# Performance work log

Hardware: AMD Instinct MI355X
Metric: run time of the kernel (lower is better)

The kernel has to match this reference:

```python
import jax, jax.numpy as jnp
import numpy as np

N = 10000       # nodes
E = 640000      # edges
D_IN = 128
D_OUT = 128
EPS = 1e-5      # LayerNorm eps (torch default)


def setup_inputs() -> dict:
    key = jax.random.key(0)
    k_x, k_e, k_w, k_b, k_g = jax.random.split(key, 5)
    x = jax.random.normal(k_x, (N, D_IN), dtype=jnp.float32)
    edge_index = jax.random.randint(k_e, (2, E), 0, N, dtype=jnp.int64)
    # GCNConv linear weight (PyG uses glorot) and bias
    lim = float(np.sqrt(6.0 / (D_IN + D_OUT)))
    W = jax.random.uniform(k_w, (D_IN, D_OUT), minval=-lim, maxval=lim, dtype=jnp.float32)
    b = jnp.zeros((D_OUT,), dtype=jnp.float32)
    # LayerNorm affine params
    gamma = jnp.ones((D_OUT,), dtype=jnp.float32)
    beta = jnp.zeros((D_OUT,), dtype=jnp.float32)
    return {"x": x, "edge_index": edge_index, "W": W, "b": b, "gamma": gamma, "beta": beta}


def reference(x, edge_index, W, b, gamma, beta):
    # --- GCNConv: A_hat = D^{-1/2} (A + I) D^{-1/2}; out = A_hat X W + b ---
    self_idx = jnp.arange(N, dtype=edge_index.dtype)
    src = jnp.concatenate([edge_index[0], self_idx])  # [E+N]
    dst = jnp.concatenate([edge_index[1], self_idx])  # [E+N]
    deg = jax.ops.segment_sum(jnp.ones_like(src, dtype=x.dtype), dst, num_segments=N)
    dinv = jnp.where(deg > 0, jax.lax.rsqrt(deg), 0.0)  # [N]
    norm = dinv[src] * dinv[dst]                        # [E+N]
    h = x @ W                                           # [N, D_OUT] transform first (cheaper)
    msg = h[src] * norm[:, None]                        # [E+N, D_OUT]
    out = jax.ops.segment_sum(msg, dst, num_segments=N) + b
    # --- LayerNorm over feature dim ---
    mu = jnp.mean(out, axis=-1, keepdims=True)
    var = jnp.mean(jnp.square(out - mu), axis=-1, keepdims=True)
    out = (out - mu) * jax.lax.rsqrt(var + EPS) * gamma + beta
    # act = Identity (last_act=ReLU is truthy -> Identity branch); dropout = eval identity; residual=False
    return out
```

## Files before the change

kernel.cpp:

```cpp
#include <hip/hip_runtime.h>
#include <hip/hip_fp16.h>

#define D 128
#define LN_EPS 1e-5f


static __device__ __forceinline__ float h2f(unsigned short h) {
    return __half2float(__builtin_bit_cast(__half, h));
}
static __device__ __forceinline__ unsigned short f2h(float f) {
    return __builtin_bit_cast(unsigned short, __float2half_rn(f));
}

static __device__ __forceinline__ void flagbar(int* slots, int c, int C, int phase) {
    __syncthreads();
    int val = 0x5A5A0001 + phase;
    int tid = threadIdx.x;
    if (tid == 0)
        __hip_atomic_store(&slots[phase * 64 + c], val, __ATOMIC_RELEASE, __HIP_MEMORY_SCOPE_AGENT);
    if (tid < C) {
        while (__hip_atomic_load(&slots[phase * 64 + tid], __ATOMIC_ACQUIRE, __HIP_MEMORY_SCOPE_AGENT) != val)
            __builtin_amdgcn_s_sleep(1);
    }
    __syncthreads();
}

__global__ __launch_bounds__(1024) void build_kernel(
        const int* __restrict__ src, const int* __restrict__ dst,
        const float* __restrict__ x, const float* __restrict__ W,
        unsigned int* __restrict__ xh, unsigned int* __restrict__ Wh,
        unsigned short* __restrict__ ghist, int* __restrict__ blocksum,
        int* __restrict__ rowptr, float* __restrict__ dinv,
        unsigned short* __restrict__ csr, int* __restrict__ bar,
        int N, int E, int Ec, int NH, int NW, int C) {
    extern __shared__ int lds[];
    __shared__ int s_scan[20];
    int c = blockIdx.x;
    int tid = threadIdx.x;
    int lane = tid & 63, wv = tid >> 6;

    for (int i = tid; i < N; i += 1024) lds[i] = 0;
    int gs = gridDim.x * 1024;
    int tot = NH + NW;
    for (int i = c * 1024 + tid; i < tot; i += gs) {
        if (i < NH) {
            float2 v = ((const float2*)x)[i];
            xh[i] = (unsigned int)f2h(v.x) | ((unsigned int)f2h(v.y) << 16);
        } else {
            float2 v = ((const float2*)W)[i - NH];
            Wh[i - NH] = (unsigned int)f2h(v.x) | ((unsigned int)f2h(v.y) << 16);
        }
    }
    __syncthreads();
    int lo = c * Ec, hi = min(lo + Ec, E);
    #pragma unroll 4
    for (int i = lo + tid; i < hi; i += 1024)
        atomicAdd(&lds[dst[i]], 1);
    __syncthreads();
    for (int i = tid; i < N; i += 1024)
        ghist[(size_t)c * N + i] = (unsigned short)lds[i];
    flagbar(bar, c, C, 0);

    int nper = (N + C - 1) / C;
    int n0 = c * nper;
    int nn = min(nper, N - n0); if (nn < 0) nn = 0;
    int mydeg = 0;
    if (tid < nn) {
        int n = n0 + tid;
        int run = 0;
        #pragma unroll 8
        for (int cc = 0; cc < C; cc++) {
            int t = ghist[(size_t)cc * N + n];
            ghist[(size_t)cc * N + n] = (unsigned short)run;
            run += t;
        }
        mydeg = run;
        dinv[n] = rsqrtf((float)(run + 1));
    }
    int incl = mydeg;
    #pragma unroll
    for (int off = 1; off < 64; off <<= 1) {
        int y = __shfl_up(incl, off);
        if (lane >= off) incl += y;
    }
    if (lane == 63) s_scan[wv] = incl;
    __syncthreads();
    if (tid == 0) {
        int run = 0;
        #pragma unroll
        for (int k = 0; k < 16; k++) { int t = s_scan[k]; s_scan[k] = run; run += t; }
        blocksum[c] = run;
    }
    __syncthreads();
    if (tid < nn) rowptr[n0 + tid] = s_scan[wv] + incl - mydeg;
    flagbar(bar, c, C, 1);

    if (tid < 64) {
        int bs = (tid < C) ? blocksum[tid] : 0;
        int inc2 = bs;
        #pragma unroll
        for (int off = 1; off < 64; off <<= 1) {
            int y = __shfl_up(inc2, off);
            if (tid >= off) inc2 += y;
        }
        if (tid == c)     s_scan[18] = inc2 - bs;
        if (tid == C - 1) s_scan[19] = inc2;
    }
    __syncthreads();
    int base = s_scan[18];
    if (tid < nn) rowptr[n0 + tid] += base;
    if (c == C - 1 && tid == 0) rowptr[N] = s_scan[19];
    flagbar(bar, c, C, 2);

    for (int i = tid; i < N; i += 1024)
        lds[i] = rowptr[i] + ghist[(size_t)c * N + i];
    __syncthreads();
    #pragma unroll 4
    for (int i = lo + tid; i < hi; i += 1024) {
        int d = dst[i];
        int pos = atomicAdd(&lds[d], 1);
        csr[pos] = (unsigned short)src[i];
    }
}

__global__ __launch_bounds__(512) void fused_fp16(const unsigned int* __restrict__ xh,
                                                  const unsigned int* __restrict__ Wh,
                                                  const int* __restrict__ rowptr,
                                                  const unsigned short* __restrict__ csr,
                                                  const float* __restrict__ dinv,
                                                  const float* __restrict__ bias,
                                                  const float* __restrict__ gamma,
                                                  const float* __restrict__ beta,
                                                  float* __restrict__ out, int N) {
    int w = threadIdx.x >> 6, lane = threadIdx.x & 63;
    int node = blockIdx.x * 8 + w;
    if (node >= N) return;
    float dn = dinv[node];

    unsigned int xv = xh[node * 64 + lane];
    float a0 = h2f((unsigned short)xv) * dn * dn;
    float a1 = h2f((unsigned short)(xv >> 16)) * dn * dn;

    int start = rowptr[node], end = rowptr[node + 1];
    int base = start;
    for (; base + 64 <= end; base += 64) {
        int s = csr[base + lane];
        float wt = dinv[s] * dn;
        #pragma unroll 8
        for (int k = 0; k < 64; k++) {
            int sk = __shfl(s, k);
            float wk = __shfl(wt, k);
            unsigned int hv = xh[sk * 64 + lane];
            a0 += h2f((unsigned short)hv) * wk;
            a1 += h2f((unsigned short)(hv >> 16)) * wk;
        }
    }
    int rem = end - base;
    if (rem > 0) {
        int s = 0; float wt = 0.f;
        if (lane < rem) { s = csr[base + lane]; wt = dinv[s] * dn; }
        for (int k = 0; k < rem; k++) {
            int sk = __shfl(s, k);
            float wk = __shfl(wt, k);
            unsigned int hv = xh[sk * 64 + lane];
            a0 += h2f((unsigned short)hv) * wk;
            a1 += h2f((unsigned short)(hv >> 16)) * wk;
        }
    }

    int c0 = lane * 2;
    float y0 = bias[c0], y1 = bias[c0 + 1];
    #pragma unroll 8
    for (int k = 0; k < 64; k++) {
        float g0 = __shfl(a0, k);
        float g1 = __shfl(a1, k);
        unsigned int w0 = Wh[(2 * k) * 64 + lane];
        unsigned int w1 = Wh[(2 * k + 1) * 64 + lane];
        y0 += g0 * h2f((unsigned short)w0) + g1 * h2f((unsigned short)w1);
        y1 += g0 * h2f((unsigned short)(w0 >> 16)) + g1 * h2f((unsigned short)(w1 >> 16));
    }

    float sum = y0 + y1, sq = y0 * y0 + y1 * y1;
    #pragma unroll
    for (int off = 32; off > 0; off >>= 1) {
        sum += __shfl_xor(sum, off);
        sq  += __shfl_xor(sq, off);
    }
    float mean = sum * (1.0f / D);
    float var  = sq * (1.0f / D) - mean * mean;
    float inv  = rsqrtf(var + LN_EPS);
    float o0 = (y0 - mean) * inv * gamma[c0] + beta[c0];
    float o1 = (y1 - mean) * inv * gamma[c0 + 1] + beta[c0 + 1];
    *(float2*)(out + (size_t)node * D + c0) = make_float2(o0, o1);
}


__global__ void deg_kernel(const int* __restrict__ dst, int* __restrict__ deg, int E) {
    int e = blockIdx.x * blockDim.x + threadIdx.x;
    if (e < E) atomicAdd(&deg[dst[e]], 1);
}
__global__ __launch_bounds__(1024) void scan_kernel(const int* __restrict__ deg,
                                                    int* __restrict__ rowptr,
                                                    int* __restrict__ fill,
                                                    float* __restrict__ dinv, int N) {
    __shared__ int s_wsum[16];
    __shared__ int s_woff[16];
    __shared__ int s_carry;
    int t = threadIdx.x;
    int lane = t & 63, w = t >> 6;
    if (t == 0) s_carry = 0;
    __syncthreads();
    for (int base = 0; base < N; base += 1024) {
        int i = base + t;
        int v = (i < N) ? deg[i] : 0;
        int incl = v;
        #pragma unroll
        for (int off = 1; off < 64; off <<= 1) {
            int y = __shfl_up(incl, off);
            if (lane >= off) incl += y;
        }
        if (lane == 63) s_wsum[w] = incl;
        __syncthreads();
        if (t == 0) {
            int run = s_carry;
            #pragma unroll
            for (int k = 0; k < 16; k++) { s_woff[k] = run; run += s_wsum[k]; }
            s_carry = run;
        }
        __syncthreads();
        if (i < N) {
            int rp = s_woff[w] + (incl - v);
            rowptr[i] = rp;
            fill[i] = rp;
            dinv[i] = rsqrtf((float)(v + 1));
        }
    }
    if (t == 0) rowptr[N] = s_carry;
}
__global__ void fill_kernel(const int* __restrict__ src, const int* __restrict__ dst,
                            int* __restrict__ fill, unsigned short* __restrict__ csr, int E) {
    int e = blockIdx.x * blockDim.x + threadIdx.x;
    if (e < E) {
        int pos = atomicAdd(&fill[dst[e]], 1);
        csr[pos] = (unsigned short)src[e];
    }
}
__global__ __launch_bounds__(512) void fused_fp32(const float* __restrict__ x,
                                                  const float* __restrict__ W,
                                                  const int* __restrict__ rowptr,
                                                  const unsigned short* __restrict__ csr,
                                                  const float* __restrict__ dinv,
                                                  const float* __restrict__ bias,
                                                  const float* __restrict__ gamma,
                                                  const float* __restrict__ beta,
                                                  float* __restrict__ out, int N) {
    __shared__ float sW[D * D];
    {
        const float4* Wv = (const float4*)W;
        float4* sWv = (float4*)sW;
        #pragma unroll
        for (int i = 0; i < (D * D / 4) / 512; i++)
            sWv[threadIdx.x + i * 512] = Wv[threadIdx.x + i * 512];
    }
    __syncthreads();
    int w = threadIdx.x >> 6, lane = threadIdx.x & 63;
    int node = blockIdx.x * 8 + w;
    if (node >= N) return;
    float dn = dinv[node];
    int c0 = lane * 2;
    float2 xv = *(const float2*)(x + (size_t)node * D + c0);
    float a0 = xv.x * dn * dn, a1 = xv.y * dn * dn;
    int start = rowptr[node], end = rowptr[node + 1];
    int base = start;
    for (; base + 64 <= end; base += 64) {
        int s = csr[base + lane];
        float wt = dinv[s] * dn;
        #pragma unroll 8
        for (int k = 0; k < 64; k++) {
            int sk = __shfl(s, k);
            float wk = __shfl(wt, k);
            float2 xs = *(const float2*)(x + (size_t)sk * D + c0);
            a0 += xs.x * wk; a1 += xs.y * wk;
        }
    }
    int rem = end - base;
    if (rem > 0) {
        int s = 0; float wt = 0.f;
        if (lane < rem) { s = csr[base + lane]; wt = dinv[s] * dn; }
        for (int k = 0; k < rem; k++) {
            int sk = __shfl(s, k);
            float wk = __shfl(wt, k);
            float2 xs = *(const float2*)(x + (size_t)sk * D + c0);
            a0 += xs.x * wk; a1 += xs.y * wk;
        }
    }
    float y0 = bias[c0], y1 = bias[c0 + 1];
    #pragma unroll 8
    for (int k = 0; k < 64; k++) {
        float g0 = __shfl(a0, k);
        float g1 = __shfl(a1, k);
        float2 w0 = *(const float2*)(sW + (2 * k) * D + c0);
        float2 w1 = *(const float2*)(sW + (2 * k + 1) * D + c0);
        y0 += g0 * w0.x + g1 * w1.x;
        y1 += g0 * w0.y + g1 * w1.y;
    }
    float sum = y0 + y1, sq = y0 * y0 + y1 * y1;
    #pragma unroll
    for (int off = 32; off > 0; off >>= 1) {
        sum += __shfl_xor(sum, off);
        sq  += __shfl_xor(sq, off);
    }
    float mean = sum * (1.0f / D);
    float var  = sq * (1.0f / D) - mean * mean;
    float inv  = rsqrtf(var + LN_EPS);
    float o0 = (y0 - mean) * inv * gamma[c0] + beta[c0];
    float o1 = (y1 - mean) * inv * gamma[c0 + 1] + beta[c0 + 1];
    *(float2*)(out + (size_t)node * D + c0) = make_float2(o0, o1);
}

extern "C" void kernel_launch(void* const* d_in, const int* in_sizes, int n_in,
                              void* d_out, int out_size, void* d_ws, size_t ws_size,
                              hipStream_t stream) {
    const float* x     = (const float*)d_in[0];
    const int*   ei    = (const int*)d_in[1];
    const float* W     = (const float*)d_in[2];
    const float* bias  = (const float*)d_in[3];
    const float* gamma = (const float*)d_in[4];
    const float* beta  = (const float*)d_in[5];
    float*       out   = (float*)d_out;

    int N = in_sizes[0] / D;
    int E = in_sizes[1] / 2;
    const int* src = ei;
    const int* dst = ei + E;

    char* ws = (char*)d_ws;
    size_t off = 0;
    auto carve = [&](size_t bytes) { size_t p = off; off = (off + bytes + 15) & ~15UL; return (void*)(ws + p); };
    int*            bar      = (int*)           carve(3 * 64 * 4);
    int*            blocksum = (int*)           carve(64 * 4);
    int*            rowptr   = (int*)           carve((size_t)(N + 1) * 4);
    float*          dinv     = (float*)         carve((size_t)N * 4);
    unsigned short* csr      = (unsigned short*)carve((size_t)E * 2);
    unsigned int*   xh       = (unsigned int*)  carve((size_t)N * (D / 2) * 4);
    unsigned int*   Wh       = (unsigned int*)  carve((size_t)D * (D / 2) * 4);
    size_t fixed_end = off;

    int C = 0;
    if (ws_size > fixed_end + 16) {
        size_t avail = ws_size - fixed_end - 16;
        size_t cmax = avail / ((size_t)N * 2);
        C = (int)((cmax > 64) ? 64 : cmax);
    }

    if (C >= 16) {
        unsigned short* ghist = (unsigned short*)carve((size_t)C * N * 2);
        int Ec = (E + C - 1) / C;
        int NH = N * (D / 2);
        int NW = D * (D / 2);
        size_t lds = (size_t)N * 4;
        build_kernel<<<C, 1024, lds, stream>>>(src, dst, x, W, xh, Wh, ghist,
                                               blocksum, rowptr, dinv, csr, bar,
                                               N, E, Ec, NH, NW, C);
        fused_fp16<<<(N + 7) / 8, 512, 0, stream>>>(xh, Wh, rowptr, csr, dinv,
                                                    bias, gamma, beta, out, N);
    } else {
        int* deg  = (int*)carve((size_t)N * 4);
        int* fill = (int*)carve((size_t)N * 4);
        hipMemsetAsync(deg, 0, (size_t)N * 4, stream);
        deg_kernel<<<(E + 255) / 256, 256, 0, stream>>>(dst, deg, E);
        scan_kernel<<<1, 1024, 0, stream>>>(deg, rowptr, fill, dinv, N);
        fill_kernel<<<(E + 255) / 256, 256, 0, stream>>>(src, dst, fill, csr, E);
        fused_fp32<<<(N + 7) / 8, 512, 0, stream>>>(x, W, rowptr, csr, dinv,
                                                    bias, gamma, beta, out, N);
    }
}
```

Measured before the change: 152.4 us.

## Replace per-block LDS histograms with global atomics across 256-block persistent grid

Rewrites the CSR build kernel to drop the per-block LDS degree histograms and the two-level distributed scan. It launches 256 blocks that count degrees with global atomics, lets a single block scan the degrees, then fills the CSR using global atomics on a fill array. The aim is to use more of the GPU in the build phase and to remove the ghist traffic and extra scan stages. In exchange it adds global-atomic contention, a serial single-block scan over N nodes, and a spin barrier across 256 blocks, which assumes all blocks are resident at once.

```diff
diff --git a/kernel.cpp b/kernel.cpp
--- a/kernel.cpp
+++ b/kernel.cpp
@@ -12,37 +12,40 @@
     return __builtin_bit_cast(unsigned short, __float2half_rn(f));
 }
 
-static __device__ __forceinline__ void flagbar(int* slots, int c, int C, int phase) {
+#define NBAR_SLOTS 256
+
+static __device__ __forceinline__ void flagbar(int* slots, int c, int G, int phase) {
     __syncthreads();
     int val = 0x5A5A0001 + phase;
     int tid = threadIdx.x;
     if (tid == 0)
-        __hip_atomic_store(&slots[phase * 64 + c], val, __ATOMIC_RELEASE, __HIP_MEMORY_SCOPE_AGENT);
-    if (tid < C) {
-        while (__hip_atomic_load(&slots[phase * 64 + tid], __ATOMIC_ACQUIRE, __HIP_MEMORY_SCOPE_AGENT) != val)
+        __hip_atomic_store(&slots[phase * NBAR_SLOTS + c], val, __ATOMIC_RELEASE, __HIP_MEMORY_SCOPE_AGENT);
+    if (tid < G) {
+        while (__hip_atomic_load(&slots[phase * NBAR_SLOTS + tid], __ATOMIC_ACQUIRE, __HIP_MEMORY_SCOPE_AGENT) != val)
             __builtin_amdgcn_s_sleep(1);
     }
     __syncthreads();
 }
 
-__global__ __launch_bounds__(1024) void build_kernel(
+__global__ __launch_bounds__(1024) void build2_kernel(
         const int* __restrict__ src, const int* __restrict__ dst,
         const float* __restrict__ x, const float* __restrict__ W,
         unsigned int* __restrict__ xh, unsigned int* __restrict__ Wh,
-        unsigned short* __restrict__ ghist, int* __restrict__ blocksum,
-        int* __restrict__ rowptr, float* __restrict__ dinv,
+        int* __restrict__ deg, int* __restrict__ rowptr,
+        int* __restrict__ fill, float* __restrict__ dinv,
         unsigned short* __restrict__ csr, int* __restrict__ bar,
-        int N, int E, int Ec, int NH, int NW, int C) {
-    extern __shared__ int lds[];
-    __shared__ int s_scan[20];
+        int N, int E, int NH, int NW, int G) {
+    __shared__ int s_wsum[16];
+    __shared__ int s_woff[16];
+    __shared__ int s_carry;
     int c = blockIdx.x;
     int tid = threadIdx.x;
-    int lane = tid & 63, wv = tid >> 6;
-
-    for (int i = tid; i < N; i += 1024) lds[i] = 0;
-    int gs = gridDim.x * 1024;
+    int gs = G * 1024;
+    int g0 = c * 1024 + tid;
+
+    for (int i = g0; i < N; i += gs) deg[i] = 0;
     int tot = NH + NW;
-    for (int i = c * 1024 + tid; i < tot; i += gs) {
+    for (int i = g0; i < tot; i += gs) {
         if (i < NH) {
             float2 v = ((const float2*)x)[i];
             xh[i] = (unsigned int)f2h(v.x) | ((unsigned int)f2h(v.y) << 16);
@@ -51,74 +54,50 @@
             Wh[i - NH] = (unsigned int)f2h(v.x) | ((unsigned int)f2h(v.y) << 16);
         }
     }
-    __syncthreads();
-    int lo = c * Ec, hi = min(lo + Ec, E);
-    #pragma unroll 4
-    for (int i = lo + tid; i < hi; i += 1024)
-        atomicAdd(&lds[dst[i]], 1);
-    __syncthreads();
-    for (int i = tid; i < N; i += 1024)
-        ghist[(size_t)c * N + i] = (unsigned short)lds[i];
-    flagbar(bar, c, C, 0);
-
-    int nper = (N + C - 1) / C;
-    int n0 = c * nper;
-    int nn = min(nper, N - n0); if (nn < 0) nn = 0;
-    int mydeg = 0;
-    if (tid < nn) {
-        int n = n0 + tid;
-        int run = 0;
-        #pragma unroll 8
-        for (int cc = 0; cc < C; cc++) {
-            int t = ghist[(size_t)cc * N + n];
-            ghist[(size_t)cc * N + n] = (unsigned short)run;
-            run += t;
-        }
-        mydeg = run;
-        dinv[n] = rsqrtf((float)(run + 1));
-    }
-    int incl = mydeg;
-    #pragma unroll
-    for (int off = 1; off < 64; off <<= 1) {
-        int y = __shfl_up(incl, off);
-        if (lane >= off) incl += y;
-    }
-    if (lane == 63) s_scan[wv] = incl;
-    __syncthreads();
-    if (tid == 0) {
-        int run = 0;
-        #pragma unroll
-        for (int k = 0; k < 16; k++) { int t = s_scan[k]; s_scan[k] = run; run += t; }
-        blocksum[c] = run;
-    }
-    __syncthreads();
-    if (tid < nn) rowptr[n0 + tid] = s_scan[wv] + incl - mydeg;
-    flagbar(bar, c, C, 1);
-
-    if (tid < 64) {
-        int bs = (tid < C) ? blocksum[tid] : 0;
-        int inc2 = bs;
-        #pragma unroll
-        for (int off = 1; off < 64; off <<= 1) {
-            int y = __shfl_up(inc2, off);
-            if (tid >= off) inc2 += y;
-        }
-        if (tid == c)     s_scan[18] = inc2 - bs;
-        if (tid == C - 1) s_scan[19] = inc2;
-    }
-    __syncthreads();
-    int base = s_scan[18];
-    if (tid < nn) rowptr[n0 + tid] += base;
-    if (c == C - 1 && tid == 0) rowptr[N] = s_scan[19];
-    flagbar(bar, c, C, 2);
-
-    for (int i = tid; i < N; i += 1024)
-        lds[i] = rowptr[i] + ghist[(size_t)c * N + i];
-    __syncthreads();
-    #pragma unroll 4
-    for (int i = lo + tid; i < hi; i += 1024) {
-        int d = dst[i];
-        int pos = atomicAdd(&lds[d], 1);
+    flagbar(bar, c, G, 0);
+
+    #pragma unroll 2
+    for (int i = g0; i < E; i += gs)
+        atomicAdd(&deg[dst[i]], 1);
+    flagbar(bar, c, G, 1);
+
+    if (c == 0) {
+        int lane = tid & 63, w = tid >> 6;
+        if (tid == 0) s_carry = 0;
+        __syncthreads();
+        for (int base = 0; base < N; base += 1024) {
+            int i = base + tid;
+            int v = (i < N) ? deg[i] : 0;
+            int incl = v;
+            #pragma unroll
+            for (int off = 1; off < 64; off <<= 1) {
+                int y = __shfl_up(incl, off);
+                if (lane >= off) incl += y;
+            }
+            if (lane == 63) s_wsum[w] = incl;
+            __syncthreads();
+            if (tid == 0) {
+                int run = s_carry;
+                #pragma unroll
+                for (int k = 0; k < 16; k++) { s_woff[k] = run; run += s_wsum[k]; }
+                s_carry = run;
+            }
+            __syncthreads();
+            if (i < N) {
+                int rp = s_woff[w] + (incl - v);
+                rowptr[i] = rp;
+                fill[i] = rp;
+                dinv[i] = rsqrtf((float)(v + 1));
+            }
+        }
+        if (tid == 0) rowptr[N] = s_carry;
+    }
+    flagbar(bar, c, G, 2);
+
+    #pragma unroll 2
+    for (int i = g0; i < E; i += gs) {
+        int d_ = dst[i];
+        int pos = atomicAdd(&fill[d_], 1);
         csr[pos] = (unsigned short)src[i];
     }
 }
@@ -337,36 +316,27 @@
     char* ws = (char*)d_ws;
     size_t off = 0;
     auto carve = [&](size_t bytes) { size_t p = off; off = (off + bytes + 15) & ~15UL; return (void*)(ws + p); };
-    int*            bar      = (int*)           carve(3 * 64 * 4);
-    int*            blocksum = (int*)           carve(64 * 4);
-    int*            rowptr   = (int*)           carve((size_t)(N + 1) * 4);
-    float*          dinv     = (float*)         carve((size_t)N * 4);
-    unsigned short* csr      = (unsigned short*)carve((size_t)E * 2);
-    unsigned int*   xh       = (unsigned int*)  carve((size_t)N * (D / 2) * 4);
-    unsigned int*   Wh       = (unsigned int*)  carve((size_t)D * (D / 2) * 4);
-    size_t fixed_end = off;
-
-    int C = 0;
-    if (ws_size > fixed_end + 16) {
-        size_t avail = ws_size - fixed_end - 16;
-        size_t cmax = avail / ((size_t)N * 2);
-        C = (int)((cmax > 64) ? 64 : cmax);
-    }
-
-    if (C >= 16) {
-        unsigned short* ghist = (unsigned short*)carve((size_t)C * N * 2);
-        int Ec = (E + C - 1) / C;
+    int*            bar    = (int*)           carve(3 * NBAR_SLOTS * 4);
+    int*            rowptr = (int*)           carve((size_t)(N + 1) * 4);
+    float*          dinv   = (float*)         carve((size_t)N * 4);
+    int*            deg    = (int*)           carve((size_t)N * 4);
+    int*            fill   = (int*)           carve((size_t)N * 4);
+    unsigned short* csr    = (unsigned short*)carve((size_t)E * 2);
+    size_t fallback_end = off;
+    unsigned int*   xh     = (unsigned int*)  carve((size_t)N * (D / 2) * 4);
+    unsigned int*   Wh     = (unsigned int*)  carve((size_t)D * (D / 2) * 4);
+    size_t full_end = off;
+
+    if (full_end <= ws_size && N <= 65535) {
+        int G = 256;
         int NH = N * (D / 2);
         int NW = D * (D / 2);
-        size_t lds = (size_t)N * 4;
-        build_kernel<<<C, 1024, lds, stream>>>(src, dst, x, W, xh, Wh, ghist,
-                                               blocksum, rowptr, dinv, csr, bar,
-                                               N, E, Ec, NH, NW, C);
+        build2_kernel<<<G, 1024, 0, stream>>>(src, dst, x, W, xh, Wh,
+                                              deg, rowptr, fill, dinv, csr, bar,
+                                              N, E, NH, NW, G);
         fused_fp16<<<(N + 7) / 8, 512, 0, stream>>>(xh, Wh, rowptr, csr, dinv,
                                                     bias, gamma, beta, out, N);
-    } else {
-        int* deg  = (int*)carve((size_t)N * 4);
-        int* fill = (int*)carve((size_t)N * 4);
+    } else if (fallback_end <= ws_size) {
         hipMemsetAsync(deg, 0, (size_t)N * 4, stream);
         deg_kernel<<<(E + 255) / 256, 256, 0, stream>>>(dst, deg, E);
         scan_kernel<<<1, 1024, 0, stream>>>(deg, rowptr, fill, dinv, N);
```

Result: slower. 281.0 us (+84.5%).

## Transform features before aggregation and fold source normalization into prescaled H

Applied to the files above, without the earlier changes.

The dense transform now runs first, as a separate GEMM kernel that computes H = X·W, scales each row by dinv[src] and stores it as fp16. The aggregation kernel then just sums the prescaled H rows over the CSR neighbors and multiplies by dinv[dst]. This removes the per-edge dinv gather and multiply and drops the per-node GEMM from the fused kernel. The costs are an extra kernel launch, an fp16 round trip of H, and rounding after the product instead of before it.

```diff
diff --git a/kernel.cpp b/kernel.cpp
--- a/kernel.cpp
+++ b/kernel.cpp
@@ -27,12 +27,11 @@
 
 __global__ __launch_bounds__(1024) void build_kernel(
         const int* __restrict__ src, const int* __restrict__ dst,
-        const float* __restrict__ x, const float* __restrict__ W,
-        unsigned int* __restrict__ xh, unsigned int* __restrict__ Wh,
+        const float* __restrict__ W, unsigned int* __restrict__ Wh,
         unsigned short* __restrict__ ghist, int* __restrict__ blocksum,
         int* __restrict__ rowptr, float* __restrict__ dinv,
         unsigned short* __restrict__ csr, int* __restrict__ bar,
-        int N, int E, int Ec, int NH, int NW, int C) {
+        int N, int E, int Ec, int NW, int C) {
     extern __shared__ int lds[];
     __shared__ int s_scan[20];
     int c = blockIdx.x;
@@ -41,15 +40,9 @@
 
     for (int i = tid; i < N; i += 1024) lds[i] = 0;
     int gs = gridDim.x * 1024;
-    int tot = NH + NW;
-    for (int i = c * 1024 + tid; i < tot; i += gs) {
-        if (i < NH) {
-            float2 v = ((const float2*)x)[i];
-            xh[i] = (unsigned int)f2h(v.x) | ((unsigned int)f2h(v.y) << 16);
-        } else {
-            float2 v = ((const float2*)W)[i - NH];
-            Wh[i - NH] = (unsigned int)f2h(v.x) | ((unsigned int)f2h(v.y) << 16);
-        }
+    for (int i = c * 1024 + tid; i < NW; i += gs) {
+        float2 v = ((const float2*)W)[i];
+        Wh[i] = (unsigned int)f2h(v.x) | ((unsigned int)f2h(v.y) << 16);
     }
     __syncthreads();
     int lo = c * Ec, hi = min(lo + Ec, E);
@@ -123,62 +116,75 @@
     }
 }
 
-__global__ __launch_bounds__(512) void fused_fp16(const unsigned int* __restrict__ xh,
+__global__ __launch_bounds__(1024) void gemm_half(const float* __restrict__ x,
                                                   const unsigned int* __restrict__ Wh,
-                                                  const int* __restrict__ rowptr,
-                                                  const unsigned short* __restrict__ csr,
                                                   const float* __restrict__ dinv,
-                                                  const float* __restrict__ bias,
-                                                  const float* __restrict__ gamma,
-                                                  const float* __restrict__ beta,
-                                                  float* __restrict__ out, int N) {
+                                                  unsigned int* __restrict__ Hh,
+                                                  int N) {
+    int wv = threadIdx.x >> 6, lane = threadIdx.x & 63;
+    int gw = blockIdx.x * 16 + wv;
+    int totw = gridDim.x * 16;
+    for (int r = gw; r < N; r += totw) {
+        float2 xr = ((const float2*)x)[r * 64 + lane];
+        float y0 = 0.f, y1 = 0.f;
+        #pragma unroll 8
+        for (int k = 0; k < 64; k++) {
+            float g0 = __shfl(xr.x, k);
+            float g1 = __shfl(xr.y, k);
+            unsigned int w0 = Wh[(2 * k) * 64 + lane];
+            unsigned int w1 = Wh[(2 * k + 1) * 64 + lane];
+            y0 += g0 * h2f((unsigned short)w0) + g1 * h2f((unsigned short)w1);
+            y1 += g0 * h2f((unsigned short)(w0 >> 16)) + g1 * h2f((unsigned short)(w1 >> 16));
+        }
+        float dr = dinv[r];
+        Hh[r * 64 + lane] = (unsigned int)f2h(y0 * dr) | ((unsigned int)f2h(y1 * dr) << 16);
+    }
+}
+
+__global__ __launch_bounds__(512) void fused_agg(const unsigned int* __restrict__ Hh,
+                                                 const int* __restrict__ rowptr,
+                                                 const unsigned short* __restrict__ csr,
+                                                 const float* __restrict__ dinv,
+                                                 const float* __restrict__ bias,
+                                                 const float* __restrict__ gamma,
+                                                 const float* __restrict__ beta,
+                                                 float* __restrict__ out, int N) {
     int w = threadIdx.x >> 6, lane = threadIdx.x & 63;
     int node = blockIdx.x * 8 + w;
     if (node >= N) return;
     float dn = dinv[node];
 
-    unsigned int xv = xh[node * 64 + lane];
-    float a0 = h2f((unsigned short)xv) * dn * dn;
-    float a1 = h2f((unsigned short)(xv >> 16)) * dn * dn;
+    unsigned int hv0 = Hh[node * 64 + lane];
+    float a0 = h2f((unsigned short)hv0);
+    float a1 = h2f((unsigned short)(hv0 >> 16));
 
     int start = rowptr[node], end = rowptr[node + 1];
     int base = start;
     for (; base + 64 <= end; base += 64) {
         int s = csr[base + lane];
-        float wt = dinv[s] * dn;
         #pragma unroll 8
         for (int k = 0; k < 64; k++) {
             int sk = __shfl(s, k);
-            float wk = __shfl(wt, k);
-            unsigned int hv = xh[sk * 64 + lane];
-            a0 += h2f((unsigned short)hv) * wk;
-            a1 += h2f((unsigned short)(hv >> 16)) * wk;
+            unsigned int hv = Hh[sk * 64 + lane];
+            a0 += h2f((unsigned short)hv);
+            a1 += h2f((unsigned short)(hv >> 16));
         }
     }
     int rem = end - base;
     if (rem > 0) {
-        int s = 0; float wt = 0.f;
-        if (lane < rem) { s = csr[base + lane]; wt = dinv[s] * dn; }
+        int s = 0;
+        if (lane < rem) s = csr[base + lane];
         for (int k = 0; k < rem; k++) {
             int sk = __shfl(s, k);
-            float wk = __shfl(wt, k);
-            unsigned int hv = xh[sk * 64 + lane];
-            a0 += h2f((unsigned short)hv) * wk;
-            a1 += h2f((unsigned short)(hv >> 16)) * wk;
+            unsigned int hv = Hh[sk * 64 + lane];
+            a0 += h2f((unsigned short)hv);
+            a1 += h2f((unsigned short)(hv >> 16));
         }
     }
 
     int c0 = lane * 2;
-    float y0 = bias[c0], y1 = bias[c0 + 1];
-    #pragma unroll 8
-    for (int k = 0; k < 64; k++) {
-        float g0 = __shfl(a0, k);
-        float g1 = __shfl(a1, k);
-        unsigned int w0 = Wh[(2 * k) * 64 + lane];
-        unsigned int w1 = Wh[(2 * k + 1) * 64 + lane];
-        y0 += g0 * h2f((unsigned short)w0) + g1 * h2f((unsigned short)w1);
-        y1 += g0 * h2f((unsigned short)(w0 >> 16)) + g1 * h2f((unsigned short)(w1 >> 16));
-    }
+    float y0 = dn * a0 + bias[c0];
+    float y1 = dn * a1 + bias[c0 + 1];
 
     float sum = y0 + y1, sq = y0 * y0 + y1 * y1;
     #pragma unroll
@@ -342,7 +348,7 @@
     int*            rowptr   = (int*)           carve((size_t)(N + 1) * 4);
     float*          dinv     = (float*)         carve((size_t)N * 4);
     unsigned short* csr      = (unsigned short*)carve((size_t)E * 2);
-    unsigned int*   xh       = (unsigned int*)  carve((size_t)N * (D / 2) * 4);
+    unsigned int*   Hh       = (unsigned int*)  carve((size_t)N * (D / 2) * 4);
     unsigned int*   Wh       = (unsigned int*)  carve((size_t)D * (D / 2) * 4);
     size_t fixed_end = off;
 
@@ -353,17 +359,17 @@
         C = (int)((cmax > 64) ? 64 : cmax);
     }
 
-    if (C >= 16) {
+    if (C >= 16 && N <= 65535) {
         unsigned short* ghist = (unsigned short*)carve((size_t)C * N * 2);
         int Ec = (E + C - 1) / C;
-        int NH = N * (D / 2);
         int NW = D * (D / 2);
         size_t lds = (size_t)N * 4;
-        build_kernel<<<C, 1024, lds, stream>>>(src, dst, x, W, xh, Wh, ghist,
+        build_kernel<<<C, 1024, lds, stream>>>(src, dst, W, Wh, ghist,
                                                blocksum, rowptr, dinv, csr, bar,
-                                               N, E, Ec, NH, NW, C);
-        fused_fp16<<<(N + 7) / 8, 512, 0, stream>>>(xh, Wh, rowptr, csr, dinv,
-                                                    bias, gamma, beta, out, N);
+                                               N, E, Ec, NW, C);
+        gemm_half<<<256, 1024, 0, stream>>>(x, Wh, dinv, Hh, N);
+        fused_agg<<<(N + 7) / 8, 512, 0, stream>>>(Hh, rowptr, csr, dinv,
+                                                   bias, gamma, beta, out, N);
     } else {
         int* deg  = (int*)carve((size_t)N * 4);
         int* fill = (int*)carve((size_t)N * 4);
```

Measured after the change: 153.5 us. Within noise of the previous version (+0.7%).
